# Kernel tuning notes

Hardware: AMD Instinct MI355X
Metric: run time of the kernel (lower is better)

## Reference

```python
import jax, jax.numpy as jnp
import numpy as np

NUM_CLASSES = 2
IGNORE_INDEX = 2


def setup_inputs() -> dict:
    key = jax.random.key(0)
    k1, k2 = jax.random.split(key)
    probs = jax.random.uniform(k1, (2, 2, 32, 512, 512), dtype=jnp.float32)  # (B,C,D,H,W)
    gt_mask = jax.random.randint(k2, (2, 32, 512, 512), 0, 3, dtype=jnp.int32)  # (B,D,H,W), includes ignore_index=2
    return {"probs": probs, "gt_mask": gt_mask}


def _one_hot_target(gt_mask):
    # ignore_index -> 0, clamp to [0, NUM_CLASSES-1], one-hot to channel axis 1
    gt = jnp.where(gt_mask == IGNORE_INDEX, 0, gt_mask)
    gt = jnp.clip(gt, 0, NUM_CLASSES - 1)
    oh = jax.nn.one_hot(gt, NUM_CLASSES, dtype=jnp.float32)  # (B,D,H,W,C)
    return jnp.moveaxis(oh, -1, 1)  # (B,C,D,H,W)


def reference(probs, gt_mask):
    # Per-z-slice 2D loss (surrogate for the opaque topological _loss_2d:
    # mean squared error between probs and one-hot target per slice),
    # vectorized over the z loop, then 'mean' reduction over slices.
    oh = _one_hot_target(gt_mask)  # (B,C,D,H,W)
    per_z = jnp.mean((probs - oh) ** 2, axis=(0, 1, 3, 4))  # (D,)
    return jnp.mean(per_z)
```

## Files before the change

kernel.cpp:

```cpp
#include <hip/hip_runtime.h>

static constexpr long long DHW       = 32LL * 512 * 512;
static constexpr long long N_SPATIAL = 2LL * DHW;
static constexpr long long N_TOTAL   = 2LL * N_SPATIAL;

static constexpr int GRID  = 2048;
static constexpr int BLOCK = 256;
static constexpr long long NVEC   = N_SPATIAL / 4;
static constexpr long long STRIDE = (long long)GRID * BLOCK;
static_assert(NVEC == 8 * STRIDE, "exact 8 iterations per thread");

__device__ __forceinline__ float chunk_mse(const float* __restrict__ probs,
                                           const int*   __restrict__ mask,
                                           long long v) {
    const long long s    = v << 2;
    const long long b    = s >> 23;
    const long long rest = s & (DHW - 1);
    const long long base = (b << 24) + rest;

    const float4 p0 = *reinterpret_cast<const float4*>(probs + base);
    const float4 p1 = *reinterpret_cast<const float4*>(probs + base + DHW);
    const int4   m  = *reinterpret_cast<const int4*>(mask + s);

    const float t0 = (m.x == 1) ? 1.0f : 0.0f;
    const float t1 = (m.y == 1) ? 1.0f : 0.0f;
    const float t2 = (m.z == 1) ? 1.0f : 0.0f;
    const float t3 = (m.w == 1) ? 1.0f : 0.0f;

    float acc = 0.0f, d;
    d = p0.x - (1.0f - t0); acc += d * d;
    d = p0.y - (1.0f - t1); acc += d * d;
    d = p0.z - (1.0f - t2); acc += d * d;
    d = p0.w - (1.0f - t3); acc += d * d;
    d = p1.x - t0;          acc += d * d;
    d = p1.y - t1;          acc += d * d;
    d = p1.z - t2;          acc += d * d;
    d = p1.w - t3;          acc += d * d;
    return acc;
}

__global__ __launch_bounds__(BLOCK) void betti_mse_partial(const float* __restrict__ probs,
                                                           const int*   __restrict__ mask,
                                                           double*      __restrict__ partial) {
    const long long v0 = (long long)blockIdx.x * BLOCK + threadIdx.x;
    float acc0 = 0.0f, acc1 = 0.0f;
    #pragma unroll
    for (int i = 0; i < 4; ++i) {
        acc0 += chunk_mse(probs, mask, v0 + (2 * i + 0) * STRIDE);
        acc1 += chunk_mse(probs, mask, v0 + (2 * i + 1) * STRIDE);
    }
    float local = acc0 + acc1;

    #pragma unroll
    for (int off = 32; off > 0; off >>= 1)
        local += __shfl_down(local, off, 64);

    __shared__ float wsum[4];
    const int lane = threadIdx.x & 63;
    const int wid  = threadIdx.x >> 6;
    if (lane == 0) wsum[wid] = local;
    __syncthreads();
    if (threadIdx.x == 0)
        partial[blockIdx.x] = (double)(wsum[0] + wsum[1] + wsum[2] + wsum[3]);
}

__global__ __launch_bounds__(BLOCK) void betti_mse_final(const double* __restrict__ partial,
                                                         float* __restrict__ out) {
    double local = 0.0;
    #pragma unroll
    for (int k = 0; k < GRID / BLOCK; ++k)
        local += partial[threadIdx.x + k * BLOCK];

    #pragma unroll
    for (int off = 32; off > 0; off >>= 1)
        local += __shfl_down(local, off, 64);

    __shared__ double wsum[4];
    const int lane = threadIdx.x & 63;
    const int wid  = threadIdx.x >> 6;
    if (lane == 0) wsum[wid] = local;
    __syncthreads();
    if (threadIdx.x == 0)
        out[0] = (float)((wsum[0] + wsum[1] + wsum[2] + wsum[3]) / (double)N_TOTAL);
}

extern "C" void kernel_launch(void* const* d_in, const int* in_sizes, int n_in,
                              void* d_out, int out_size, void* d_ws, size_t ws_size,
                              hipStream_t stream) {
    const float* probs   = (const float*)d_in[0];
    const int*   mask    = (const int*)d_in[1];
    float*       out     = (float*)d_out;
    double*      partial = (double*)d_ws;

    betti_mse_partial<<<GRID, BLOCK, 0, stream>>>(probs, mask, partial);
    betti_mse_final<<<1, BLOCK, 0, stream>>>(partial, out);
}
```

Baseline: 234.1 us.

## Stream inputs through LDS with async global_load_lds double buffering

Replaces direct vector global loads with 16-byte global-to-LDS async loads into per-wave double buffers, so the next round's loads are in flight while the current round is consumed. Waits use hand-coded s_waitcnt vmcnt values rather than barriers, which relies on per-wave LDS segments and on exact in-order counting of vm operations. Grid is halved with twice as many rounds per thread. The goal is more memory-level parallelism on a bandwidth-bound reduction, at the cost of LDS usage and fragile wait encodings.

```diff
diff --git a/kernel.cpp b/kernel.cpp
--- a/kernel.cpp
+++ b/kernel.cpp
@@ -1,66 +1,91 @@
 #include <hip/hip_runtime.h>
+#include <stdint.h>
 
 static constexpr long long DHW       = 32LL * 512 * 512;
 static constexpr long long N_SPATIAL = 2LL * DHW;
 static constexpr long long N_TOTAL   = 2LL * N_SPATIAL;
 
-static constexpr int GRID  = 2048;
-static constexpr int BLOCK = 256;
-static constexpr long long NVEC   = N_SPATIAL / 4;
-static constexpr long long STRIDE = (long long)GRID * BLOCK;
-static_assert(NVEC == 8 * STRIDE, "exact 8 iterations per thread");
+static constexpr int GRID   = 1024;
+static constexpr int BLOCK  = 256;
+static constexpr int ROUNDS = 16;
+static constexpr long long CHUNKS  = N_SPATIAL / 4;
+static constexpr long long RSTRIDE = (long long)GRID * BLOCK;
+static_assert(CHUNKS == (long long)ROUNDS * RSTRIDE, "exact trip count");
 
-__device__ __forceinline__ float chunk_mse(const float* __restrict__ probs,
-                                           const int*   __restrict__ mask,
-                                           long long v) {
-    const long long s    = v << 2;
-    const long long b    = s >> 23;
-    const long long rest = s & (DHW - 1);
-    const long long base = (b << 24) + rest;
+typedef float fx4 __attribute__((ext_vector_type(4)));
+typedef int   ix4 __attribute__((ext_vector_type(4)));
 
-    const float4 p0 = *reinterpret_cast<const float4*>(probs + base);
-    const float4 p1 = *reinterpret_cast<const float4*>(probs + base + DHW);
-    const int4   m  = *reinterpret_cast<const int4*>(mask + s);
-
-    const float t0 = (m.x == 1) ? 1.0f : 0.0f;
-    const float t1 = (m.y == 1) ? 1.0f : 0.0f;
-    const float t2 = (m.z == 1) ? 1.0f : 0.0f;
-    const float t3 = (m.w == 1) ? 1.0f : 0.0f;
-
-    float acc = 0.0f, d;
-    d = p0.x - (1.0f - t0); acc += d * d;
-    d = p0.y - (1.0f - t1); acc += d * d;
-    d = p0.z - (1.0f - t2); acc += d * d;
-    d = p0.w - (1.0f - t3); acc += d * d;
-    d = p1.x - t0;          acc += d * d;
-    d = p1.y - t1;          acc += d * d;
-    d = p1.z - t2;          acc += d * d;
-    d = p1.w - t3;          acc += d * d;
-    return acc;
+__device__ __forceinline__ void stage16(const void* g, void* lds) {
+    __builtin_amdgcn_global_load_lds(
+        (const __attribute__((address_space(1))) void*)g,
+        (__attribute__((address_space(3))) void*)lds,
+        16, 0, 0);
 }
 
 __global__ __launch_bounds__(BLOCK) void betti_mse_partial(const float* __restrict__ probs,
                                                            const int*   __restrict__ mask,
                                                            double*      __restrict__ partial) {
-    const long long v0 = (long long)blockIdx.x * BLOCK + threadIdx.x;
-    float acc0 = 0.0f, acc1 = 0.0f;
-    #pragma unroll
-    for (int i = 0; i < 4; ++i) {
-        acc0 += chunk_mse(probs, mask, v0 + (2 * i + 0) * STRIDE);
-        acc1 += chunk_mse(probs, mask, v0 + (2 * i + 1) * STRIDE);
+    __shared__ float lp0[2][BLOCK * 4];
+    __shared__ float lp1[2][BLOCK * 4];
+    __shared__ int   lm [2][BLOCK * 4];
+
+    const int tid  = threadIdx.x;
+    const int wseg = (tid >> 6) << 8;
+
+    float a0 = 0.0f, a1 = 0.0f;
+
+    auto stage = [&](int buf, int r) {
+        const long long v    = (long long)r * RSTRIDE + (long long)blockIdx.x * BLOCK + tid;
+        const long long s    = v << 2;
+        const long long b    = s >> 23;
+        const long long base = (b << 24) + (s & (DHW - 1));
+        stage16(probs + base,       &lp0[buf][wseg]);
+        stage16(probs + base + DHW, &lp1[buf][wseg]);
+        stage16(mask + s,           &lm [buf][wseg]);
+    };
+
+    auto consume = [&](int buf) {
+        const fx4 p0 = *reinterpret_cast<const fx4*>(&lp0[buf][tid << 2]);
+        const fx4 p1 = *reinterpret_cast<const fx4*>(&lp1[buf][tid << 2]);
+        const ix4 m  = *reinterpret_cast<const ix4*>(&lm [buf][tid << 2]);
+        const float t0 = (m.x == 1) ? 1.0f : 0.0f;
+        const float t1 = (m.y == 1) ? 1.0f : 0.0f;
+        const float t2 = (m.z == 1) ? 1.0f : 0.0f;
+        const float t3 = (m.w == 1) ? 1.0f : 0.0f;
+        float d;
+        d = p0.x - (1.0f - t0); a0 += d * d;
+        d = p0.y - (1.0f - t1); a1 += d * d;
+        d = p0.z - (1.0f - t2); a0 += d * d;
+        d = p0.w - (1.0f - t3); a1 += d * d;
+        d = p1.x - t0;          a0 += d * d;
+        d = p1.y - t1;          a1 += d * d;
+        d = p1.z - t2;          a0 += d * d;
+        d = p1.w - t3;          a1 += d * d;
+    };
+
+    stage(0, 0);
+    for (int r = 0; r < ROUNDS - 1; ++r) {
+        stage((r + 1) & 1, r + 1);
+        __builtin_amdgcn_s_waitcnt(0x0F73);
+        __asm__ __volatile__("" ::: "memory");
+        consume(r & 1);
+        __asm__ __volatile__("" ::: "memory");
     }
-    float local = acc0 + acc1;
+    __builtin_amdgcn_s_waitcnt(0x0F70);
+    __asm__ __volatile__("" ::: "memory");
+    consume((ROUNDS - 1) & 1);
 
+    float local = a0 + a1;
     #pragma unroll
     for (int off = 32; off > 0; off >>= 1)
         local += __shfl_down(local, off, 64);
 
     __shared__ float wsum[4];
-    const int lane = threadIdx.x & 63;
-    const int wid  = threadIdx.x >> 6;
+    const int lane = tid & 63;
+    const int wid  = tid >> 6;
     if (lane == 0) wsum[wid] = local;
     __syncthreads();
-    if (threadIdx.x == 0)
+    if (tid == 0)
         partial[blockIdx.x] = (double)(wsum[0] + wsum[1] + wsum[2] + wsum[3]);
 }
 
```

Measured after the change: 231.3 us. About the same (-1.2%).
